# Optimization experiments

Hardware: AMD Instinct MI355X
Metric: run time of the kernel (lower is better)

Reference implementation:

```python
import jax, jax.numpy as jnp
import numpy as np

N_NODES = 10000
N_EDGES = 80000
IN_DIM = 768
HID = 256
HEADS = 8
NEG_SLOPE = 0.2


def setup_inputs() -> dict:
    key = jax.random.key(0)
    ks = jax.random.split(key, 12)
    s = 0.02
    x = jax.random.normal(ks[0], (N_NODES, IN_DIM), dtype=jnp.float32)
    edge_index = jax.random.randint(ks[1], (2, N_EDGES), 0, N_NODES, dtype=jnp.int64)
    W1 = jax.random.normal(ks[2], (IN_DIM, HEADS * HID), dtype=jnp.float32) * s
    a_src1 = jax.random.normal(ks[3], (HEADS, HID), dtype=jnp.float32) * s
    a_dst1 = jax.random.normal(ks[4], (HEADS, HID), dtype=jnp.float32) * s
    b1 = jnp.zeros((HEADS * HID,), dtype=jnp.float32)
    W2 = jax.random.normal(ks[5], (HEADS * HID, HEADS * HID), dtype=jnp.float32) * s
    a_src2 = jax.random.normal(ks[6], (HEADS, HID), dtype=jnp.float32) * s
    a_dst2 = jax.random.normal(ks[7], (HEADS, HID), dtype=jnp.float32) * s
    b2 = jnp.zeros((HID,), dtype=jnp.float32)
    # graph_projection: 256 -> 256
    Wp = jax.random.normal(ks[8], (HID, HID), dtype=jnp.float32) * s
    bp = jnp.zeros((HID,), dtype=jnp.float32)
    return dict(x=x, edge_index=edge_index, W1=W1, a_src1=a_src1, a_dst1=a_dst1,
                b1=b1, W2=W2, a_src2=a_src2, a_dst2=a_dst2, b2=b2, Wp=Wp, bp=bp)


def _gat_conv(x, src, dst, W, a_src, a_dst, b, concat):
    """PyG GATConv (eval mode, self-loops already appended to src/dst)."""
    N = x.shape[0]
    H, C = a_src.shape
    h = (x @ W).reshape(N, H, C)                         # [N,H,C] per-head projection
    alpha_s = jnp.sum(h * a_src[None], axis=-1)           # [N,H]
    alpha_d = jnp.sum(h * a_dst[None], axis=-1)           # [N,H]
    e = jax.nn.leaky_relu(alpha_s[src] + alpha_d[dst], NEG_SLOPE)  # [E,H]
    # segment softmax over incoming edges of each dst node
    m = jax.ops.segment_max(e, dst, num_segments=N)       # [N,H]
    m = jnp.where(jnp.isfinite(m), m, 0.0)
    p = jnp.exp(e - m[dst])
    denom = jax.ops.segment_sum(p, dst, num_segments=N)   # [N,H]
    alpha = p / (denom[dst] + 1e-16)                      # [E,H]
    out = jax.ops.segment_sum(alpha[:, :, None] * h[src], dst, num_segments=N)  # [N,H,C]
    if concat:
        return out.reshape(N, H * C) + b
    return out.mean(axis=1) + b


def reference(x, edge_index, W1, a_src1, a_dst1, b1, W2, a_src2, a_dst2, b2, Wp, bp):
    N = x.shape[0]
    loops = jnp.arange(N, dtype=edge_index.dtype)
    src = jnp.concatenate([edge_index[0], loops])
    dst = jnp.concatenate([edge_index[1], loops])
    h = _gat_conv(x, src, dst, W1, a_src1, a_dst1, b1, concat=True)   # [N, 2048]
    h = jax.nn.elu(h)                                                 # dropout: eval/no-op
    h = _gat_conv(h, src, dst, W2, a_src2, a_dst2, b2, concat=False)  # [N, 256]
    h = h @ Wp + bp
    return jax.nn.relu(h)                                             # dropout: eval/no-op
```

## Files before the change

kernel.cpp:

```cpp
#include <hip/hip_runtime.h>
#include <cstdint>
#include <cstddef>

#define IN_DIM  768
#define NNODES  10000
#define MPAD    10240
#define NEDGES  80000
#define E_TOT   90000
#define HEADS   8
#define HID     256
#define HC      2048
#define NEG_SLOPE 0.2f

#define CVT_BLK  ((MPAD * IN_DIM / 4) / 256)
#define CNT_BLK  ((E_TOT + 255) / 256)
#define T1_BLK   ((HC / 32) * (IN_DIM / 32))
#define T2_BLK   ((HC / 32) * (HC / 32))
#define TP_BLK   ((HID / 32) * (HID / 32))
#define PREP_BLK (CVT_BLK + CNT_BLK + T1_BLK + T2_BLK + TP_BLK)

typedef _Float16 __attribute__((ext_vector_type(8))) f16x8;
typedef float    __attribute__((ext_vector_type(4))) f32x4;

__device__ __forceinline__ int edge_src(const int* __restrict__ ei, int e) {
    return (e < NEDGES) ? ei[e] : (e - NEDGES);
}
__device__ __forceinline__ int edge_dst(const int* __restrict__ ei, int e) {
    return (e < NEDGES) ? ei[NEDGES + e] : (e - NEDGES);
}

__device__ __forceinline__ void tcvt_body(
    const float* __restrict__ W, _Float16* __restrict__ T,
    int K, int N, int bx, int by, int t)
{
    __shared__ float tile[32][33];
    int tx = t & 31, ty = t >> 5;
#pragma unroll
    for (int q = 0; q < 4; q++)
        tile[ty + q * 8][tx] = W[(size_t)(by * 32 + ty + q * 8) * N + bx * 32 + tx];
    __syncthreads();
#pragma unroll
    for (int q = 0; q < 4; q++) {
        float v = tile[tx][ty + q * 8];
        T[(size_t)(bx * 32 + ty + q * 8) * K + by * 32 + tx] = (_Float16)v;
    }
}

__global__ __launch_bounds__(256) void prep_kernel(
    const float* __restrict__ x, _Float16* __restrict__ xh,
    const int* __restrict__ ei, int* __restrict__ cnt,
    const float* __restrict__ W1, _Float16* __restrict__ W1t,
    const float* __restrict__ W2, _Float16* __restrict__ W2t,
    const float* __restrict__ Wp, _Float16* __restrict__ Wpt)
{
    int b = blockIdx.x;
    int t = threadIdx.x;
    if (b < CVT_BLK) {
        int i = b * 256 + t;
        size_t e = (size_t)i * 4;
        int r = (int)(e / IN_DIM);
        float4 v = (r < NNODES) ? *(const float4*)(x + e)
                                : make_float4(0.f, 0.f, 0.f, 0.f);
        _Float16 h4[4] = {(_Float16)v.x, (_Float16)v.y, (_Float16)v.z, (_Float16)v.w};
        *(ushort4*)(xh + e) = *(ushort4*)h4;
    } else if (b < CVT_BLK + CNT_BLK) {
        int e = (b - CVT_BLK) * 256 + t;
        if (e < E_TOT) atomicAdd(&cnt[edge_dst(ei, e)], 1);
    } else if (b < CVT_BLK + CNT_BLK + T1_BLK) {
        int idx = b - (CVT_BLK + CNT_BLK);
        tcvt_body(W1, W1t, IN_DIM, HC, idx % (HC / 32), idx / (HC / 32), t);
    } else if (b < CVT_BLK + CNT_BLK + T1_BLK + T2_BLK) {
        int idx = b - (CVT_BLK + CNT_BLK + T1_BLK);
        tcvt_body(W2, W2t, HC, HC, idx % (HC / 32), idx / (HC / 32), t);
    } else {
        int idx = b - (CVT_BLK + CNT_BLK + T1_BLK + T2_BLK);
        tcvt_body(Wp, Wpt, HID, HID, idx % (HID / 32), idx / (HID / 32), t);
    }
}

__global__ void scan_kernel(const int* __restrict__ cnt, int* __restrict__ indptr) {
    __shared__ int sums[1024];
    const int CH = 10;
    int t = threadIdx.x;
    int base = t * CH;
    int s = 0;
#pragma unroll
    for (int i = 0; i < CH; i++) { int idx = base + i; if (idx < NNODES) s += cnt[idx]; }
    sums[t] = s;
    __syncthreads();
    for (int off = 1; off < 1024; off <<= 1) {
        int v = (t >= off) ? sums[t - off] : 0;
        __syncthreads();
        sums[t] += v;
        __syncthreads();
    }
    int run = (t == 0) ? 0 : sums[t - 1];
#pragma unroll
    for (int i = 0; i < CH; i++) {
        int idx = base + i;
        if (idx < NNODES) { indptr[idx] = run; run += cnt[idx]; }
    }
    if (t == 0) indptr[NNODES] = E_TOT;
}

__global__ void scatter_kernel(const int* __restrict__ ei, const int* __restrict__ indptr,
                               int* __restrict__ cur, int* __restrict__ sorted) {
    int e = blockIdx.x * 256 + threadIdx.x;
    if (e < E_TOT) {
        int d = edge_dst(ei, e);
        int pos = atomicAdd(&cur[d], 1);
        sorted[indptr[d] + pos] = e;
    }
}

__global__ __launch_bounds__(512, 2) void gemm8p_kernel(
    const _Float16* __restrict__ A, const _Float16* __restrict__ B,
    _Float16* __restrict__ C, int M, int K, int Nn,
    const float* __restrict__ asrc, const float* __restrict__ adst,
    float* __restrict__ as_out, float* __restrict__ ad_out)
{
    __shared__ __align__(16) _Float16 lds[2][36864];

    const int t = threadIdx.x;
    const int w = t >> 6, lane = t & 63;
    const int fr = lane & 15, q4 = lane >> 4;
    const int wr = w >> 2, wc = w & 3;

    const int nwgx = gridDim.x;
    int wg = blockIdx.y * nwgx + blockIdx.x;
    const int cpx = (nwgx * gridDim.y) >> 3;
    wg = (wg & 7) * cpx + (wg >> 3);
    const int row0 = (wg / nwgx) * 320;
    const int col0 = (wg % nwgx) * 256;

    const int rowt = t >> 3;
    const int scol = ((t & 7) ^ (rowt & 7)) << 3;
    const _Float16* baseA = A + (size_t)(row0 + rowt) * K + scol;
    const _Float16* baseB = B + (size_t)(col0 + rowt) * K + scol;
    const int dstw = w * 512;

    auto stageA = [&](int q, int kel, int bb) {
        __builtin_amdgcn_global_load_lds(
            (const __attribute__((address_space(1))) void*)(baseA + (size_t)q * 64 * K + kel),
            (__attribute__((address_space(3))) void*)&lds[bb][q * 4096 + dstw], 16, 0, 0);
    };
    auto stageB = [&](int q, int kel, int bb) {
        __builtin_amdgcn_global_load_lds(
            (const __attribute__((address_space(1))) void*)(baseB + (size_t)q * 64 * K + kel),
            (__attribute__((address_space(3))) void*)&lds[bb][20480 + q * 4096 + dstw], 16, 0, 0);
    };

    f32x4 acc[2][2][5][2];
#pragma unroll
    for (int qm = 0; qm < 2; qm++)
#pragma unroll
        for (int qn = 0; qn < 2; qn++)
#pragma unroll
            for (int mi = 0; mi < 5; mi++)
#pragma unroll
                for (int ni = 0; ni < 2; ni++)
                    acc[qm][qn][mi][ni] = {0.f, 0.f, 0.f, 0.f};

    f16x8 fa[5][2], fb[2][2][2];

#define LOADA(BB, QM)                                                           \
    {                                                                           \
        _Pragma("unroll")                                                       \
        for (int mi = 0; mi < 5; mi++) {                                        \
            _Pragma("unroll")                                                   \
            for (int ks = 0; ks < 2; ks++) {                                    \
                int lr = wr * 80 + mi * 16 + fr;                                \
                int sl = ((ks << 2) | q4) ^ (fr & 7);                           \
                fa[mi][ks] = *(const f16x8*)&lds[BB][(QM) * 10240 + (lr << 6) + (sl << 3)]; \
            }                                                                   \
        }                                                                       \
    }
#define LOADB(BB, QN)                                                           \
    {                                                                           \
        _Pragma("unroll")                                                       \
        for (int ni = 0; ni < 2; ni++) {                                        \
            _Pragma("unroll")                                                   \
            for (int ks = 0; ks < 2; ks++) {                                    \
                int lr = wc * 32 + ni * 16 + fr;                                \
                int sl = ((ks << 2) | q4) ^ (fr & 7);                           \
                fb[QN][ni][ks] = *(const f16x8*)&lds[BB][20480 + (QN) * 8192 + (lr << 6) + (sl << 3)]; \
            }                                                                   \
        }                                                                       \
    }

#define PHASE(QM, QN, LOAD_STMT, STAGE_STMT, WAIT_STMT)                         \
    do {                                                                        \
        WAIT_STMT;                                                              \
        __builtin_amdgcn_s_barrier();                                           \
        LOAD_STMT;                                                              \
        STAGE_STMT;                                                             \
        asm volatile("s_waitcnt lgkmcnt(0)" ::: "memory");                      \
        __builtin_amdgcn_sched_barrier(0);                                      \
        __builtin_amdgcn_s_setprio(1);                                          \
        _Pragma("unroll")                                                       \
        for (int ks = 0; ks < 2; ks++) {                                        \
            _Pragma("unroll")                                                   \
            for (int mi = 0; mi < 5; mi++) {                                    \
                _Pragma("unroll")                                               \
                for (int ni = 0; ni < 2; ni++)                                  \
                    acc[QM][QN][mi][ni] = __builtin_amdgcn_mfma_f32_16x16x32_f16(\
                        fa[mi][ks], fb[QN][ni][ks], acc[QM][QN][mi][ni], 0, 0, 0); \
            }                                                                   \
        }                                                                       \
        __builtin_amdgcn_s_setprio(0);                                          \
        __builtin_amdgcn_sched_barrier(0);                                      \
    } while (0)

#define VM(N) asm volatile("s_waitcnt vmcnt(" #N ")" ::: "memory")

    stageA(0, 0, 0); stageA(1, 0, 0); stageA(2, 0, 0);
    stageB(0, 0, 0); stageB(1, 0, 0);
    stageB(2, 0, 0); stageB(3, 0, 0);
    stageA(3, 0, 0); stageA(4, 0, 0);

    const int nT = K >> 6;
    int t0 = 0;
    for (; t0 < nT - 1; ++t0) {
        int bb = t0 & 1;
        int bn = bb ^ 1;
        int k1 = (t0 + 1) << 6;
        PHASE(0, 0, { LOADA(bb, 0); LOADB(bb, 0); },
              { stageA(0, k1, bn); stageA(1, k1, bn); stageA(2, k1, bn); },
              VM(4));
        PHASE(0, 1, { LOADB(bb, 1); },
              { stageB(0, k1, bn); stageB(1, k1, bn); },
              VM(5));
        PHASE(1, 1, { LOADA(bb, 1); },
              { stageB(2, k1, bn); stageB(3, k1, bn); },
              VM(5));
        PHASE(1, 0, { },
              { stageA(3, k1, bn); stageA(4, k1, bn); },
              ((void)0));
    }
    {
        int bb = t0 & 1;
        PHASE(0, 0, { LOADA(bb, 0); LOADB(bb, 0); }, ((void)0), VM(4));
        PHASE(0, 1, { LOADB(bb, 1); },               ((void)0), VM(2));
        PHASE(1, 1, { LOADA(bb, 1); },               ((void)0), VM(0));
        PHASE(1, 0, { },                             ((void)0), ((void)0));
    }
#undef PHASE
#undef LOADA
#undef LOADB
#undef VM

#pragma unroll
    for (int qm = 0; qm < 2; qm++)
#pragma unroll
        for (int qn = 0; qn < 2; qn++)
#pragma unroll
            for (int mi = 0; mi < 5; mi++) {
                int mb = row0 + qm * 160 + wr * 80 + mi * 16 + q4 * 4;
#pragma unroll
                for (int ni = 0; ni < 2; ni++) {
                    int n = col0 + qn * 128 + wc * 32 + ni * 16 + fr;
#pragma unroll
                    for (int r = 0; r < 4; r++) {
                        int m = mb + r;
                        if (m < M) C[(size_t)m * Nn + n] = (_Float16)acc[qm][qn][mi][ni][r];
                    }
                }
            }

    if (as_out) {
        __syncthreads();
        float* sAs = (float*)&lds[0][0];
        float* sAd = sAs + 320 * 4;
        float asv[2][2], adv[2][2];
#pragma unroll
        for (int qn = 0; qn < 2; qn++)
#pragma unroll
            for (int ni = 0; ni < 2; ni++) {
                int n = col0 + qn * 128 + wc * 32 + ni * 16 + fr;
                asv[qn][ni] = asrc[n];
                adv[qn][ni] = adst[n];
            }
#pragma unroll
        for (int qm = 0; qm < 2; qm++)
#pragma unroll
            for (int mi = 0; mi < 5; mi++)
#pragma unroll
                for (int r = 0; r < 4; r++) {
                    float sa = 0.f, sd = 0.f;
#pragma unroll
                    for (int qn = 0; qn < 2; qn++)
#pragma unroll
                        for (int ni = 0; ni < 2; ni++) {
                            float v = acc[qm][qn][mi][ni][r];
                            sa = fmaf(v, asv[qn][ni], sa);
                            sd = fmaf(v, adv[qn][ni], sd);
                        }
#pragma unroll
                    for (int o = 1; o < 16; o <<= 1) {
                        sa += __shfl_xor(sa, o, 16);
                        sd += __shfl_xor(sd, o, 16);
                    }
                    if (fr == 0) {
                        int rl = qm * 160 + wr * 80 + mi * 16 + q4 * 4 + r;
                        sAs[rl * 4 + wc] = sa;
                        sAd[rl * 4 + wc] = sd;
                    }
                }
        __syncthreads();
        if (t < 320) {
            float sa = sAs[t * 4] + sAs[t * 4 + 1] + sAs[t * 4 + 2] + sAs[t * 4 + 3];
            float sd = sAd[t * 4] + sAd[t * 4 + 1] + sAd[t * 4 + 2] + sAd[t * 4 + 3];
            int m = row0 + t;
            if (m < M) {
                int head = col0 >> 8;
                as_out[m * HEADS + head] = sa;
                ad_out[m * HEADS + head] = sd;
            }
        }
    }
}

template <int EPI>
__global__ __launch_bounds__(256) void mfma_gemm_kernel(
    const _Float16* __restrict__ A, const _Float16* __restrict__ B,
    void* __restrict__ Cout, const float* __restrict__ bias,
    int M, int K, int Nn, int swz)
{
    __shared__ __align__(16) _Float16 sA[2][128 * 32];
    __shared__ __align__(16) _Float16 sB[2][128 * 32];

    int t = threadIdx.x;
    int bx = blockIdx.x, by = blockIdx.y;
    if (swz) {
        int id = by * 16 + bx;
        int xcd = id & 7, slot = id >> 3;
        bx = 2 * xcd + (slot & 1);
        by = slot >> 1;
    }
    int row0 = by * 128;
    int col0 = bx * 128;

    int s0 = t, s1 = t + 256;
    int m0 = s0 >> 2, k0 = (s0 & 3) * 8;
    int m1 = s1 >> 2, k1 = (s1 & 3) * 8;
    const _Float16* a0 = A + (size_t)(row0 + m0) * K + k0;
    const _Float16* a1 = A + (size_t)(row0 + m1) * K + k1;
    const _Float16* b0 = B + (size_t)(col0 + m0) * K + k0;
    const _Float16* b1 = B + (size_t)(col0 + m1) * K + k1;

    int w = t >> 6, lane = t & 63;
    int wm = (w & 1) * 64, wn = (w >> 1) * 64;
    int fr = lane & 15, quad = lane >> 4;

    auto stage = [&](int kt, int bsel) {
        _Float16* dA0 = &sA[bsel][(w * 64) * 8];
        _Float16* dA1 = &sA[bsel][(w * 64 + 256) * 8];
        _Float16* dB0 = &sB[bsel][(w * 64) * 8];
        _Float16* dB1 = &sB[bsel][(w * 64 + 256) * 8];
        __builtin_amdgcn_global_load_lds(
            (const __attribute__((address_space(1))) void*)(a0 + kt),
            (__attribute__((address_space(3))) void*)dA0, 16, 0, 0);
        __builtin_amdgcn_global_load_lds(
            (const __attribute__((address_space(1))) void*)(a1 + kt),
            (__attribute__((address_space(3))) void*)dA1, 16, 0, 0);
        __builtin_amdgcn_global_load_lds(
            (const __attribute__((address_space(1))) void*)(b0 + kt),
            (__attribute__((address_space(3))) void*)dB0, 16, 0, 0);
        __builtin_amdgcn_global_load_lds(
            (const __attribute__((address_space(1))) void*)(b1 + kt),
            (__attribute__((address_space(3))) void*)dB1, 16, 0, 0);
    };

    f32x4 acc[4][4];
#pragma unroll
    for (int i = 0; i < 4; i++)
#pragma unroll
        for (int j = 0; j < 4; j++) acc[i][j] = {0.f, 0.f, 0.f, 0.f};

    const int nIt = K / 32;
    stage(0, 0);
    __syncthreads();

    for (int it = 0; it < nIt; ++it) {
        int cb = it & 1;
        if (it + 1 < nIt) stage((it + 1) * 32, cb ^ 1);

        f16x8 fa[4], fb[4];
#pragma unroll
        for (int i = 0; i < 4; i++) {
            fa[i] = *(const f16x8*)&sA[cb][(wm + i * 16 + fr) * 32 + quad * 8];
            fb[i] = *(const f16x8*)&sB[cb][(wn + i * 16 + fr) * 32 + quad * 8];
        }
#pragma unroll
        for (int i = 0; i < 4; i++)
#pragma unroll
            for (int j = 0; j < 4; j++)
                acc[i][j] = __builtin_amdgcn_mfma_f32_16x16x32_f16(fa[i], fb[j], acc[i][j], 0, 0, 0);

        if (it + 1 < nIt) __syncthreads();
    }

    if (EPI == 0) {
        _Float16* C = (_Float16*)Cout;
#pragma unroll
        for (int i = 0; i < 4; i++) {
            int mbase = row0 + wm + i * 16 + quad * 4;
#pragma unroll
            for (int j = 0; j < 4; j++) {
                int n = col0 + wn + j * 16 + fr;
#pragma unroll
                for (int r = 0; r < 4; r++) {
                    int m = mbase + r;
                    if (m < M) C[(size_t)m * Nn + n] = (_Float16)acc[i][j][r];
                }
            }
        }
    } else {
        float* C = (float*)Cout;
        float bv[4];
#pragma unroll
        for (int j = 0; j < 4; j++) bv[j] = bias[col0 + wn + j * 16 + fr];
#pragma unroll
        for (int i = 0; i < 4; i++) {
            int mbase = row0 + wm + i * 16 + quad * 4;
#pragma unroll
            for (int j = 0; j < 4; j++) {
                int n = col0 + wn + j * 16 + fr;
#pragma unroll
                for (int r = 0; r < 4; r++) {
                    int m = mbase + r;
                    if (m < M) C[(size_t)m * Nn + n] = fmaxf(acc[i][j][r] + bv[j], 0.f);
                }
            }
        }
    }
}

template <int MODE>
__global__ __launch_bounds__(256) void agg_kernel(
    const _Float16* __restrict__ H, const float* __restrict__ as_,
    const float* __restrict__ ad_, const float* __restrict__ bias,
    const int* __restrict__ indptr, const int* __restrict__ sorted,
    const int* __restrict__ ei, _Float16* __restrict__ outh)
{
    __shared__ float m8[HEADS], d8[HEADS], adl[HEADS];
    __shared__ int   srcl[64];
    __shared__ float al2[HEADS][64];
    __shared__ float red[HC];

    int n = blockIdx.x;
    int t = threadIdx.x;

    if (n >= NNODES) {
        if (MODE == 0) {
            _Float16 z8[8] = {};
            *(f16x8*)&outh[(size_t)n * HC + t * 8] = *(f16x8*)z8;
        } else {
            outh[(size_t)n * HID + t] = (_Float16)0.f;
        }
        return;
    }

    int start = indptr[n];
    int deg = indptr[n + 1] - start;

    if (t < HEADS) adl[t] = ad_[n * HEADS + t];
    __syncthreads();

    int hh = t >> 5, c8 = (t & 31) * 8;
    const size_t hoff = (size_t)hh * HID + c8;
    float acc[8] = {};

    if (deg <= 64) {
        if (t < deg) srcl[t] = edge_src(ei, sorted[start + t]);
        __syncthreads();
        {
            int j = t & 63, h0 = t >> 6;
            if (j < deg) {
                int s = srcl[j];
#pragma unroll
                for (int q = 0; q < 2; q++) {
                    int hx = h0 + q * 4;
                    float v = as_[s * HEADS + hx] + adl[hx];
                    v = (v >= 0.f) ? v : NEG_SLOPE * v;
                    al2[hx][j] = v;
                }
            }
        }
        __syncthreads();
        {
            int h = t >> 5, l = t & 31;
            float mx = -1e30f;
            for (int jj = l; jj < deg; jj += 32) mx = fmaxf(mx, al2[h][jj]);
#pragma unroll
            for (int o = 16; o > 0; o >>= 1) mx = fmaxf(mx, __shfl_xor(mx, o, 32));
            float sm = 0.f;
            for (int jj = l; jj < deg; jj += 32) {
                float e = expf(al2[h][jj] - mx);
                al2[h][jj] = e;
                sm += e;
            }
#pragma unroll
            for (int o = 16; o > 0; o >>= 1) sm += __shfl_xor(sm, o, 32);
            float den = sm + 1e-16f;
            for (int jj = l; jj < deg; jj += 32) al2[h][jj] = al2[h][jj] / den;
        }
        __syncthreads();
        int jj = 0;
        for (; jj + 3 < deg; jj += 4) {
            int sx0 = srcl[jj + 0], sx1 = srcl[jj + 1];
            int sx2 = srcl[jj + 2], sx3 = srcl[jj + 3];
            f16x8 h0v = *(const f16x8*)&H[(size_t)sx0 * HC + hoff];
            f16x8 h1v = *(const f16x8*)&H[(size_t)sx1 * HC + hoff];
            f16x8 h2v = *(const f16x8*)&H[(size_t)sx2 * HC + hoff];
            f16x8 h3v = *(const f16x8*)&H[(size_t)sx3 * HC + hoff];
            float4 a4 = *(const float4*)&al2[hh][jj];
#pragma unroll
            for (int q = 0; q < 8; q++) acc[q] = fmaf(a4.x, (float)h0v[q], acc[q]);
#pragma unroll
            for (int q = 0; q < 8; q++) acc[q] = fmaf(a4.y, (float)h1v[q], acc[q]);
#pragma unroll
            for (int q = 0; q < 8; q++) acc[q] = fmaf(a4.z, (float)h2v[q], acc[q]);
#pragma unroll
            for (int q = 0; q < 8; q++) acc[q] = fmaf(a4.w, (float)h3v[q], acc[q]);
        }
        for (; jj < deg; jj++) {
            int s = srcl[jj];
            f16x8 hv = *(const f16x8*)&H[(size_t)s * HC + hoff];
            float a = al2[hh][jj];
#pragma unroll
            for (int q = 0; q < 8; q++)
                acc[q] = fmaf(a, (float)hv[q], acc[q]);
        }
    } else {
        int h = t >> 5, l = t & 31;
        float adh = adl[h];

        float mx = -1e30f;
        for (int j = l; j < deg; j += 32) {
            int e = sorted[start + j];
            int s = edge_src(ei, e);
            float v = as_[s * HEADS + h] + adh;
            v = (v >= 0.f) ? v : NEG_SLOPE * v;
            mx = fmaxf(mx, v);
        }
#pragma unroll
        for (int o = 16; o > 0; o >>= 1) mx = fmaxf(mx, __shfl_xor(mx, o, 32));

        float sm = 0.f;
        for (int j = l; j < deg; j += 32) {
            int e = sorted[start + j];
            int s = edge_src(ei, e);
            float v = as_[s * HEADS + h] + adh;
            v = (v >= 0.f) ? v : NEG_SLOPE * v;
            sm += expf(v - mx);
        }
#pragma unroll
        for (int o = 16; o > 0; o >>= 1) sm += __shfl_xor(sm, o, 32);
        if (l == 0) { m8[h] = mx; d8[h] = sm; }

        for (int base = 0; base < deg; base += 64) {
            int cntc = min(64, deg - base);
            __syncthreads();
            if (t < cntc) srcl[t] = edge_src(ei, sorted[start + base + t]);
            __syncthreads();
            {
                int j = t & 63, h0 = t >> 6;
                if (j < cntc) {
                    int s = srcl[j];
#pragma unroll
                    for (int q = 0; q < 2; q++) {
                        int hx = h0 + q * 4;
                        float v = as_[s * HEADS + hx] + adl[hx];
                        v = (v >= 0.f) ? v : NEG_SLOPE * v;
                        al2[hx][j] = expf(v - m8[hx]) / (d8[hx] + 1e-16f);
                    }
                }
            }
            __syncthreads();
            int jj = 0;
            for (; jj + 3 < cntc; jj += 4) {
                int sx0 = srcl[jj + 0], sx1 = srcl[jj + 1];
                int sx2 = srcl[jj + 2], sx3 = srcl[jj + 3];
                f16x8 h0v = *(const f16x8*)&H[(size_t)sx0 * HC + hoff];
                f16x8 h1v = *(const f16x8*)&H[(size_t)sx1 * HC + hoff];
                f16x8 h2v = *(const f16x8*)&H[(size_t)sx2 * HC + hoff];
                f16x8 h3v = *(const f16x8*)&H[(size_t)sx3 * HC + hoff];
                float4 a4 = *(const float4*)&al2[hh][jj];
#pragma unroll
                for (int q = 0; q < 8; q++) acc[q] = fmaf(a4.x, (float)h0v[q], acc[q]);
#pragma unroll
                for (int q = 0; q < 8; q++) acc[q] = fmaf(a4.y, (float)h1v[q], acc[q]);
#pragma unroll
                for (int q = 0; q < 8; q++) acc[q] = fmaf(a4.z, (float)h2v[q], acc[q]);
#pragma unroll
                for (int q = 0; q < 8; q++) acc[q] = fmaf(a4.w, (float)h3v[q], acc[q]);
            }
            for (; jj < cntc; jj++) {
                int s = srcl[jj];
                f16x8 hv = *(const f16x8*)&H[(size_t)s * HC + hoff];
                float a = al2[hh][jj];
#pragma unroll
                for (int q = 0; q < 8; q++)
                    acc[q] = fmaf(a, (float)hv[q], acc[q]);
            }
        }
    }

    if (MODE == 0) {
        _Float16 o8[8];
#pragma unroll
        for (int q = 0; q < 8; q++) {
            float v = acc[q] + bias[hoff + q];
            v = (v > 0.f) ? v : expm1f(v);
            o8[q] = (_Float16)v;
        }
        *(f16x8*)&outh[(size_t)n * HC + hoff] = *(f16x8*)o8;
    } else {
#pragma unroll
        for (int q = 0; q < 8; q++) red[hoff + q] = acc[q];
        __syncthreads();
        float s = 0.f;
#pragma unroll
        for (int h2 = 0; h2 < HEADS; h2++) s += red[h2 * HID + t];
        outh[(size_t)n * HID + t] = (_Float16)(s * 0.125f + bias[t]);
    }
}

extern "C" void kernel_launch(void* const* d_in, const int* in_sizes, int n_in,
                              void* d_out, int out_size, void* d_ws, size_t ws_size,
                              hipStream_t stream)
{
    const float* x      = (const float*)d_in[0];
    const int*   ei     = (const int*)  d_in[1];
    const float* W1     = (const float*)d_in[2];
    const float* a_src1 = (const float*)d_in[3];
    const float* a_dst1 = (const float*)d_in[4];
    const float* b1     = (const float*)d_in[5];
    const float* W2     = (const float*)d_in[6];
    const float* a_src2 = (const float*)d_in[7];
    const float* a_dst2 = (const float*)d_in[8];
    const float* b2     = (const float*)d_in[9];
    const float* Wp     = (const float*)d_in[10];
    const float* bp     = (const float*)d_in[11];
    float* out = (float*)d_out;

    char* ws = (char*)d_ws;
    size_t off = 0;
    auto alloc = [&](size_t bytes) -> char* {
        char* p = ws + off;
        off += (bytes + 255) & ~(size_t)255;
        return p;
    };
    _Float16* Hbuf = (_Float16*)alloc((size_t)NNODES * HC * 2);
    _Float16* A2   = (_Float16*)alloc((size_t)MPAD * HC * 2);
    _Float16* W1t  = (_Float16*)alloc((size_t)HC * IN_DIM * 2);
    _Float16* W2t  = (_Float16*)alloc((size_t)HC * HC * 2);
    _Float16* Wpt  = (_Float16*)alloc((size_t)HID * HID * 2);
    _Float16* xh   = (_Float16*)alloc((size_t)MPAD * IN_DIM * 2);
    _Float16* out2h = (_Float16*)alloc((size_t)MPAD * HID * 2);
    float* asad   = (float*)alloc((size_t)4 * NNODES * HEADS * sizeof(float));
    float* as1 = asad;
    float* ad1 = asad + (size_t)NNODES * HEADS;
    float* as2 = asad + (size_t)2 * NNODES * HEADS;
    float* ad2 = asad + (size_t)3 * NNODES * HEADS;
    int*   cntcur = (int*)alloc((size_t)2 * NNODES * sizeof(int));
    int*   cnt = cntcur;
    int*   cur = cntcur + NNODES;
    int*   indptr = (int*)  alloc((size_t)(NNODES + 1) * sizeof(int));
    int*   sorted = (int*)  alloc((size_t)E_TOT * sizeof(int));

    hipMemsetAsync(cntcur, 0, (size_t)2 * NNODES * sizeof(int), stream);
    prep_kernel<<<PREP_BLK, 256, 0, stream>>>(x, xh, ei, cnt,
                                              W1, W1t, W2, W2t, Wp, Wpt);
    scan_kernel<<<1, 1024, 0, stream>>>(cnt, indptr);
    scatter_kernel<<<(E_TOT + 255) / 256, 256, 0, stream>>>(ei, indptr, cur, sorted);

    dim3 g8(HC / 256, MPAD / 320);

    gemm8p_kernel<<<g8, 512, 0, stream>>>(xh, W1t, Hbuf, NNODES, IN_DIM, HC,
                                          a_src1, a_dst1, as1, ad1);
    agg_kernel<0><<<MPAD, 256, 0, stream>>>(Hbuf, as1, ad1, b1, indptr, sorted, ei, A2);

    gemm8p_kernel<<<g8, 512, 0, stream>>>(A2, W2t, Hbuf, NNODES, HC, HC,
                                          a_src2, a_dst2, as2, ad2);
    agg_kernel<1><<<MPAD, 256, 0, stream>>>(Hbuf, as2, ad2, b2, indptr, sorted, ei, out2h);

    dim3 gProj(HID / 128, MPAD / 128);
    mfma_gemm_kernel<1><<<gProj, 256, 0, stream>>>(out2h, Wpt, out, bp,
                                                   NNODES, HID, HID, 0);
}
```

Before: 422.1 us.

## Transpose attention logits to head-major layout and reload B fragments per phase

Stores the per-node attention scores as/ad in a head-major [HEADS][MPAD] layout instead of node-major, with coalesced writes from the GEMM epilogue and no row bound check (writes into padded rows). The aggregation kernels index the transposed arrays. The GEMM also keeps only one set of B fragments in registers and reloads B quadrant 0 from LDS in the last phase, lowering register pressure at the cost of extra LDS reads. Gathers in aggregation now hit different cache lines per head for the same source node, which may hurt locality.

```diff
diff --git a/kernel.cpp b/kernel.cpp
--- a/kernel.cpp
+++ b/kernel.cpp
@@ -117,7 +117,7 @@
     const _Float16* __restrict__ A, const _Float16* __restrict__ B,
     _Float16* __restrict__ C, int M, int K, int Nn,
     const float* __restrict__ asrc, const float* __restrict__ adst,
-    float* __restrict__ as_out, float* __restrict__ ad_out)
+    float* __restrict__ asT, float* __restrict__ adT)
 {
     __shared__ __align__(16) _Float16 lds[2][36864];
 
@@ -161,7 +161,7 @@
                 for (int ni = 0; ni < 2; ni++)
                     acc[qm][qn][mi][ni] = {0.f, 0.f, 0.f, 0.f};
 
-    f16x8 fa[5][2], fb[2][2][2];
+    f16x8 fa[5][2], fb[2][2];
 
 #define LOADA(BB, QM)                                                           \
     {                                                                           \
@@ -183,7 +183,7 @@
             for (int ks = 0; ks < 2; ks++) {                                    \
                 int lr = wc * 32 + ni * 16 + fr;                                \
                 int sl = ((ks << 2) | q4) ^ (fr & 7);                           \
-                fb[QN][ni][ks] = *(const f16x8*)&lds[BB][20480 + (QN) * 8192 + (lr << 6) + (sl << 3)]; \
+                fb[ni][ks] = *(const f16x8*)&lds[BB][20480 + (QN) * 8192 + (lr << 6) + (sl << 3)]; \
             }                                                                   \
         }                                                                       \
     }
@@ -204,7 +204,7 @@
                 _Pragma("unroll")                                               \
                 for (int ni = 0; ni < 2; ni++)                                  \
                     acc[QM][QN][mi][ni] = __builtin_amdgcn_mfma_f32_16x16x32_f16(\
-                        fa[mi][ks], fb[QN][ni][ks], acc[QM][QN][mi][ni], 0, 0, 0); \
+                        fa[mi][ks], fb[ni][ks], acc[QM][QN][mi][ni], 0, 0, 0);  \
             }                                                                   \
         }                                                                       \
         __builtin_amdgcn_s_setprio(0);                                          \
@@ -233,7 +233,7 @@
         PHASE(1, 1, { LOADA(bb, 1); },
               { stageB(2, k1, bn); stageB(3, k1, bn); },
               VM(5));
-        PHASE(1, 0, { },
+        PHASE(1, 0, { LOADB(bb, 0); },
               { stageA(3, k1, bn); stageA(4, k1, bn); },
               ((void)0));
     }
@@ -242,7 +242,7 @@
         PHASE(0, 0, { LOADA(bb, 0); LOADB(bb, 0); }, ((void)0), VM(4));
         PHASE(0, 1, { LOADB(bb, 1); },               ((void)0), VM(2));
         PHASE(1, 1, { LOADA(bb, 1); },               ((void)0), VM(0));
-        PHASE(1, 0, { },                             ((void)0), ((void)0));
+        PHASE(1, 0, { LOADB(bb, 0); },               ((void)0), ((void)0));
     }
 #undef PHASE
 #undef LOADA
@@ -267,7 +267,7 @@
                 }
             }
 
-    if (as_out) {
+    if (asT) {
         __syncthreads();
         float* sAs = (float*)&lds[0][0];
         float* sAd = sAs + 320 * 4;
@@ -310,12 +310,9 @@
         if (t < 320) {
             float sa = sAs[t * 4] + sAs[t * 4 + 1] + sAs[t * 4 + 2] + sAs[t * 4 + 3];
             float sd = sAd[t * 4] + sAd[t * 4 + 1] + sAd[t * 4 + 2] + sAd[t * 4 + 3];
-            int m = row0 + t;
-            if (m < M) {
-                int head = col0 >> 8;
-                as_out[m * HEADS + head] = sa;
-                ad_out[m * HEADS + head] = sd;
-            }
+            int head = col0 >> 8;
+            asT[(size_t)head * MPAD + row0 + t] = sa;
+            adT[(size_t)head * MPAD + row0 + t] = sd;
         }
     }
 }
@@ -438,8 +435,8 @@
 
 template <int MODE>
 __global__ __launch_bounds__(256) void agg_kernel(
-    const _Float16* __restrict__ H, const float* __restrict__ as_,
-    const float* __restrict__ ad_, const float* __restrict__ bias,
+    const _Float16* __restrict__ H, const float* __restrict__ asT,
+    const float* __restrict__ adT, const float* __restrict__ bias,
     const int* __restrict__ indptr, const int* __restrict__ sorted,
     const int* __restrict__ ei, _Float16* __restrict__ outh)
 {
@@ -464,7 +461,7 @@
     int start = indptr[n];
     int deg = indptr[n + 1] - start;
 
-    if (t < HEADS) adl[t] = ad_[n * HEADS + t];
+    if (t < HEADS) adl[t] = adT[(size_t)t * MPAD + n];
     __syncthreads();
 
     int hh = t >> 5, c8 = (t & 31) * 8;
@@ -481,7 +478,7 @@
 #pragma unroll
                 for (int q = 0; q < 2; q++) {
                     int hx = h0 + q * 4;
-                    float v = as_[s * HEADS + hx] + adl[hx];
+                    float v = asT[(size_t)hx * MPAD + s] + adl[hx];
                     v = (v >= 0.f) ? v : NEG_SLOPE * v;
                     al2[hx][j] = v;
                 }
@@ -540,7 +537,7 @@
         for (int j = l; j < deg; j += 32) {
             int e = sorted[start + j];
             int s = edge_src(ei, e);
-            float v = as_[s * HEADS + h] + adh;
+            float v = asT[(size_t)h * MPAD + s] + adh;
             v = (v >= 0.f) ? v : NEG_SLOPE * v;
             mx = fmaxf(mx, v);
         }
@@ -551,7 +548,7 @@
         for (int j = l; j < deg; j += 32) {
             int e = sorted[start + j];
             int s = edge_src(ei, e);
-            float v = as_[s * HEADS + h] + adh;
+            float v = asT[(size_t)h * MPAD + s] + adh;
             v = (v >= 0.f) ? v : NEG_SLOPE * v;
             sm += expf(v - mx);
         }
@@ -571,7 +568,7 @@
 #pragma unroll
                     for (int q = 0; q < 2; q++) {
                         int hx = h0 + q * 4;
-                        float v = as_[s * HEADS + hx] + adl[hx];
+                        float v = asT[(size_t)hx * MPAD + s] + adl[hx];
                         v = (v >= 0.f) ? v : NEG_SLOPE * v;
                         al2[hx][j] = expf(v - m8[hx]) / (d8[hx] + 1e-16f);
                     }
@@ -659,11 +656,11 @@
     _Float16* Wpt  = (_Float16*)alloc((size_t)HID * HID * 2);
     _Float16* xh   = (_Float16*)alloc((size_t)MPAD * IN_DIM * 2);
     _Float16* out2h = (_Float16*)alloc((size_t)MPAD * HID * 2);
-    float* asad   = (float*)alloc((size_t)4 * NNODES * HEADS * sizeof(float));
+    float* asad   = (float*)alloc((size_t)4 * HEADS * MPAD * sizeof(float));
     float* as1 = asad;
-    float* ad1 = asad + (size_t)NNODES * HEADS;
-    float* as2 = asad + (size_t)2 * NNODES * HEADS;
-    float* ad2 = asad + (size_t)3 * NNODES * HEADS;
+    float* ad1 = asad + (size_t)HEADS * MPAD;
+    float* as2 = asad + (size_t)2 * HEADS * MPAD;
+    float* ad2 = asad + (size_t)3 * HEADS * MPAD;
     int*   cntcur = (int*)alloc((size_t)2 * NNODES * sizeof(int));
     int*   cnt = cntcur;
     int*   cur = cntcur + NNODES;
```

Measured after the change: 402.5 us. 1.05x faster.
